# Kernel optimization log

Measured on AMD Instinct MI355X. Metric: run time of the kernel, lower is better.

Reference implementation:

```python
import jax, jax.numpy as jnp
import numpy as np

B, T, C, HS = 8, 4096, 1024, 128
BLOCK = 4096  # block_size; T == BLOCK here


def _pyr_mask(bs):
    # Faithful numpy translation of the torch 'pyr' buffer construction.
    h = bs // 2
    top = np.repeat(np.flip(np.tril(np.ones((h, h), np.float32)), axis=1), 2, axis=0)  # (bs, h)
    reps = np.array([2] * (h - 1) + [1])
    bot = np.concatenate(
        [np.zeros((1, h), np.float32),
         np.repeat(np.tril(np.ones((h, h), np.float32)), reps, axis=0)], axis=0)  # (bs, h)
    return np.concatenate([top, bot], axis=1)  # (bs, bs)


def setup_inputs() -> dict:
    key = jax.random.key(0)
    kx, kq, kk, kv = jax.random.split(key, 4)
    s = C ** -0.5
    x = jax.random.normal(kx, (B, T, C), jnp.float32)
    Wq = jax.random.normal(kq, (C, HS), jnp.float32) * s
    Wk = jax.random.normal(kk, (C, HS), jnp.float32) * s
    Wv = jax.random.normal(kv, (C, HS), jnp.float32) * s
    return {"x": x, "Wq": Wq, "Wk": Wk, "Wv": Wv}


def reference(x, Wq, Wk, Wv):
    Tlen = x.shape[1]
    start = (BLOCK - Tlen) // 2
    end = BLOCK + (-(BLOCK - Tlen)) // 2  # python floor-div, matches torch slicing
    mask = jnp.asarray(_pyr_mask(BLOCK)[:Tlen, start:end])  # (T, T) 0/1

    q = x @ Wq  # (B, T, HS)
    k = x @ Wk
    v = x @ Wv
    wei = jnp.einsum('btd,bsd->bts', q, k) * (HS ** -0.5)  # (B, T, T)
    wei = jnp.where(mask == 0, -jnp.inf, wei)  # bidirectional_mode == 'bi'
    wei = jax.nn.softmax(wei, axis=-1)
    # dropout p=0.0 -> identity
    return wei @ v  # (B, T, HS)
```

## Files before the change

### kernel.cpp

```cpp
#include <hip/hip_runtime.h>

typedef unsigned short u16;
typedef __attribute__((ext_vector_type(8))) short bf16x8;
typedef __attribute__((ext_vector_type(8))) unsigned short u16x8;
typedef __attribute__((ext_vector_type(4))) float f32x4;
typedef __attribute__((ext_vector_type(4))) unsigned short u16x4;

#define Bn 8
#define Tn 4096
#define Cn 1024
#define HSn 128

__device__ __forceinline__ float bf2f(u16 b) {
    unsigned u = ((unsigned)b) << 16;
    return __builtin_bit_cast(float, u);
}
__device__ __forceinline__ u16 f2bf(float f) {
    unsigned u = __builtin_bit_cast(unsigned, f);
    unsigned r = (u + 0x7fffu + ((u >> 16) & 1u)) >> 16;
    return (u16)r;
}

extern "C" __global__ __launch_bounds__(256) void head_wtrans(
    const float* __restrict__ Wq, const float* __restrict__ Wk,
    const float* __restrict__ Wv, u16* __restrict__ wt) {
    const float* W = (blockIdx.y == 0) ? Wq : (blockIdx.y == 1) ? Wk : Wv;
    const float scale =
        (blockIdx.y == 0) ? (0.08838834764831845f * 1.4426950408889634f) : 1.0f;
    u16* o = wt + (size_t)blockIdx.y * Cn * HSn;
    int tid = blockIdx.x * 256 + threadIdx.x;
    int n = tid >> 10, kk = tid & 1023;
    o[tid] = f2bf(W[kk * HSn + n] * scale);
}

extern "C" __global__ __launch_bounds__(256, 1) void head_proj(
    const float* __restrict__ x, const u16* __restrict__ wt, u16* __restrict__ qo,
    u16* __restrict__ ko, u16* __restrict__ vto) {
    __shared__ __align__(16) u16 aL[128 * 40];
    __shared__ __align__(16) u16 bL[3 * 128 * 40];
    const int tid = threadIdx.x;
    const int w = tid >> 6, l = tid & 63, quad = l >> 4, ln = l & 15;
    const int bm0 = blockIdx.x * 128;

    const f32x4 zero4 = {0.f, 0.f, 0.f, 0.f};
    f32x4 acc[3][4][4];
#pragma unroll
    for (int s = 0; s < 3; s++)
#pragma unroll
        for (int i = 0; i < 4; i++)
#pragma unroll
            for (int j = 0; j < 4; j++) acc[s][i][j] = zero4;

    const int m0w = (w & 1) * 64, n0w = (w >> 1) * 64;

    f32x4 xp[4];
    u16x8 wp[3][2];
    const int xrow[4] = {tid >> 3, (256 + tid) >> 3, (512 + tid) >> 3, (768 + tid) >> 3};
    const int xch = tid & 7;
    const int wrow[2] = {tid >> 2, (256 + tid) >> 2};
    const int wch = tid & 3;

#pragma unroll
    for (int p = 0; p < 4; p++)
        xp[p] = *(const f32x4*)(x + ((size_t)(bm0 + xrow[p])) * Cn + xch * 4);
#pragma unroll
    for (int s = 0; s < 3; s++)
#pragma unroll
        for (int p = 0; p < 2; p++)
            wp[s][p] = *(const u16x8*)(wt + (size_t)s * Cn * HSn + (size_t)wrow[p] * Cn +
                                       wch * 8);

    for (int kt = 0; kt < Cn / 32; kt++) {
        __syncthreads();
#pragma unroll
        for (int p = 0; p < 4; p++) {
            u16x4 vb;
#pragma unroll
            for (int j = 0; j < 4; j++) vb[j] = f2bf(xp[p][j]);
            *(u16x4*)(aL + xrow[p] * 40 + xch * 4) = vb;
        }
#pragma unroll
        for (int s = 0; s < 3; s++)
#pragma unroll
            for (int p = 0; p < 2; p++)
                *(u16x8*)(bL + s * 5120 + wrow[p] * 40 + wch * 8) = wp[s][p];
        if (kt + 1 < Cn / 32) {
            const int kn = (kt + 1) * 32;
#pragma unroll
            for (int p = 0; p < 4; p++)
                xp[p] = *(const f32x4*)(x + ((size_t)(bm0 + xrow[p])) * Cn + kn + xch * 4);
#pragma unroll
            for (int s = 0; s < 3; s++)
#pragma unroll
                for (int p = 0; p < 2; p++)
                    wp[s][p] = *(const u16x8*)(wt + (size_t)s * Cn * HSn +
                                               (size_t)wrow[p] * Cn + kn + wch * 8);
        }
        __syncthreads();
        bf16x8 af[4];
#pragma unroll
        for (int mi = 0; mi < 4; mi++)
            af[mi] = *(const bf16x8*)(aL + (m0w + mi * 16 + ln) * 40 + quad * 8);
#pragma unroll
        for (int s = 0; s < 3; s++) {
            bf16x8 bf[4];
#pragma unroll
            for (int ni = 0; ni < 4; ni++)
                bf[ni] =
                    *(const bf16x8*)(bL + s * 5120 + (n0w + ni * 16 + ln) * 40 + quad * 8);
#pragma unroll
            for (int mi = 0; mi < 4; mi++)
#pragma unroll
                for (int ni = 0; ni < 4; ni++)
                    acc[s][mi][ni] = __builtin_amdgcn_mfma_f32_16x16x32_bf16(
                        af[mi], bf[ni], acc[s][mi][ni], 0, 0, 0);
        }
    }
#pragma unroll
    for (int mi = 0; mi < 4; mi++)
#pragma unroll
        for (int ni = 0; ni < 4; ni++)
#pragma unroll
            for (int r = 0; r < 4; r++) {
                int grow = bm0 + m0w + mi * 16 + quad * 4 + r;
                int col = n0w + ni * 16 + ln;
                qo[(size_t)grow * HSn + col] = f2bf(acc[0][mi][ni][r]);
                ko[(size_t)grow * HSn + col] = f2bf(acc[1][mi][ni][r]);
                int bb = grow >> 12, t = grow & 4095;
                vto[((size_t)bb * HSn + col) * Tn + t] = f2bf(acc[2][mi][ni][r]);
            }
}


extern "C" __global__ __launch_bounds__(256) void head_flash_chunk(
    const u16* __restrict__ q, const u16* __restrict__ k, const u16* __restrict__ vt,
    u16* __restrict__ Opart, float* __restrict__ ml) {
    __shared__ __align__(16) u16 kL[64 * 136];
    __shared__ __align__(16) u16 vL[128 * 72];
    __shared__ __align__(16) u16 pL[4 * 16 * 72];
    const int tid = threadIdx.x;
    const int w = tid >> 6, l = tid & 63, quad = l >> 4, ln = l & 15;
    const int cid = blockIdx.x;
    const int qb = 63 - (cid >> 4);
    const int b = (cid & 15) >> 1;
    const int half = cid & 1;
    const int q0 = qb * 64;
    const int qrow = q0 + w * 16;

    const int rkBase = tid >> 4, ckK = tid & 15;
    const int rvBase = tid >> 3, ckV = tid & 7;

    bf16x8 qf[4];
#pragma unroll
    for (int ks = 0; ks < 4; ks++)
        qf[ks] = *(const bf16x8*)(q + ((size_t)b * Tn + qrow + ln) * HSn + ks * 32 +
                                  quad * 8);

    const f32x4 zero4 = {0.f, 0.f, 0.f, 0.f};
    float m2 = -1e30f, l2 = 0.f;
    const int qme = qrow + ln;
    const int clo = 2047 - (qme >> 1), chi = 2047 + ((qme + 1) >> 1);
    f32x4 o[8];
#pragma unroll
    for (int dt = 0; dt < 8; dt++) o[dt] = zero4;

    const int qmax = q0 + 63;
    const int tlo = (2047 - (qmax >> 1)) >> 6;
    const int thi = (2047 + ((qmax + 1) >> 1)) >> 6;
    const int W = thi - tlo + 1;
    const int c0 = (W + 1) >> 1;
    const int kstart = half ? tlo + c0 : tlo;
    const int kend = half ? thi : tlo + c0 - 1;

    u16x8 pk[4], pv[4];
    {
        const int t0 = kstart * 64;
#pragma unroll
        for (int p = 0; p < 4; p++)
            pk[p] = *(const u16x8*)(k + ((size_t)b * Tn + t0 + p * 16 + rkBase) * HSn +
                                    ckK * 8);
#pragma unroll
        for (int p = 0; p < 4; p++)
            pv[p] = *(const u16x8*)(vt + ((size_t)b * HSn + p * 32 + rvBase) * Tn + t0 +
                                    ckV * 8);
    }

    for (int kt = kstart; kt <= kend; kt++) {
        const int t0 = kt * 64;
        __syncthreads();
#pragma unroll
        for (int p = 0; p < 4; p++)
            *(u16x8*)(kL + (p * 16 + rkBase) * 136 + ckK * 8) = pk[p];
#pragma unroll
        for (int p = 0; p < 4; p++)
            *(u16x8*)(vL + (p * 32 + rvBase) * 72 + ckV * 8) = pv[p];
        if (kt < kend) {
            const int t1 = t0 + 64;
#pragma unroll
            for (int p = 0; p < 4; p++)
                pk[p] = *(const u16x8*)(k + ((size_t)b * Tn + t1 + p * 16 + rkBase) * HSn +
                                        ckK * 8);
#pragma unroll
            for (int p = 0; p < 4; p++)
                pv[p] = *(const u16x8*)(vt + ((size_t)b * HSn + p * 32 + rvBase) * Tn +
                                        t1 + ckV * 8);
        }
        __syncthreads();

        f32x4 s[4];
#pragma unroll
        for (int nt = 0; nt < 4; nt++) s[nt] = zero4;
#pragma unroll
        for (int nt = 0; nt < 4; nt++) {
            int R = nt * 16 + ln;
#pragma unroll
            for (int ks = 0; ks < 4; ks++) {
                bf16x8 kf = *(const bf16x8*)(kL + R * 136 + (ks * 4 + quad) * 8);
                s[nt] = __builtin_amdgcn_mfma_f32_16x16x32_bf16(kf, qf[ks], s[nt], 0, 0, 0);
            }
        }
#pragma unroll
        for (int nt = 0; nt < 4; nt++)
#pragma unroll
            for (int r = 0; r < 4; r++) {
                int t = t0 + nt * 16 + quad * 4 + r;
                bool valid = (t >= clo) && (t <= chi);
                s[nt][r] = valid ? s[nt][r] : -1e30f;
            }
        float mc = s[0][0];
#pragma unroll
        for (int nt = 0; nt < 4; nt++)
#pragma unroll
            for (int r = 0; r < 4; r++) mc = fmaxf(mc, s[nt][r]);
        mc = fmaxf(mc, __shfl_xor(mc, 16, 64));
        mc = fmaxf(mc, __shfl_xor(mc, 32, 64));
        float mn = fmaxf(m2, mc);
        float alpha = exp2f(m2 - mn);
        m2 = mn;
        float ls = 0.f;
#pragma unroll
        for (int nt = 0; nt < 4; nt++) {
            u16x4 pb4;
#pragma unroll
            for (int r = 0; r < 4; r++) {
                float pvx = exp2f(s[nt][r] - mn);
                u16 pb = f2bf(pvx);
                ls += bf2f(pb);
                pb4[r] = pb;
            }
            *(u16x4*)(pL + w * 1152 + ln * 72 + nt * 16 + quad * 4) = pb4;
        }
        ls += __shfl_xor(ls, 16, 64);
        ls += __shfl_xor(ls, 32, 64);
        l2 = l2 * alpha + ls;
        float aR[4];
#pragma unroll
        for (int r = 0; r < 4; r++) aR[r] = __shfl(alpha, quad * 4 + r, 64);
#pragma unroll
        for (int dt = 0; dt < 8; dt++) {
            f32x4 oo = o[dt];
#pragma unroll
            for (int r = 0; r < 4; r++) oo[r] *= aR[r];
            o[dt] = oo;
        }
#pragma unroll
        for (int jt = 0; jt < 2; jt++) {
            bf16x8 pf = *(const bf16x8*)(pL + w * 1152 + ln * 72 + jt * 32 + quad * 8);
#pragma unroll
            for (int dt = 0; dt < 8; dt++) {
                int R = dt * 16 + ln;
                bf16x8 vf = *(const bf16x8*)(vL + R * 72 + (jt * 4 + quad) * 8);
                o[dt] = __builtin_amdgcn_mfma_f32_16x16x32_bf16(pf, vf, o[dt], 0, 0, 0);
            }
        }
    }
#pragma unroll
    for (int dt = 0; dt < 8; dt++)
#pragma unroll
        for (int r = 0; r < 4; r++)
            Opart[((size_t)cid * 64 + w * 16 + quad * 4 + r) * HSn + dt * 16 + ln] =
                f2bf(o[dt][r]);
    if (l < 16) {
        ml[((size_t)cid * 64 + w * 16 + ln) * 2 + 0] = m2;
        ml[((size_t)cid * 64 + w * 16 + ln) * 2 + 1] = l2;
    }
}

extern "C" __global__ __launch_bounds__(256) void head_combine(
    const u16* __restrict__ Opart, const float* __restrict__ ml,
    float* __restrict__ out) {
    const int bid = blockIdx.x;
    const int qb = bid >> 3, b = bid & 7;
    const int tid = threadIdx.x;
    const int row = tid >> 2, dseg = (tid & 3) * 32;
    const int cid0 = (63 - qb) * 16 + b * 2;
    const size_t r0 = (size_t)cid0 * 64 + row, r1 = r0 + 64;
    float m0 = ml[r0 * 2], l0 = ml[r0 * 2 + 1];
    float m1 = ml[r1 * 2], l1 = ml[r1 * 2 + 1];
    float ms = fmaxf(m0, m1);
    float w0 = exp2f(m0 - ms), w1 = exp2f(m1 - ms);
    float inv = 1.0f / (w0 * l0 + w1 * l1);
    float* op = out + ((size_t)b * Tn + qb * 64 + row) * HSn + dseg;
    const u16* p0 = Opart + r0 * HSn + dseg;
    const u16* p1 = Opart + r1 * HSn + dseg;
#pragma unroll
    for (int j = 0; j < 4; j++) {
        u16x8 a = *(const u16x8*)(p0 + j * 8);
        u16x8 c = *(const u16x8*)(p1 + j * 8);
        f32x4 o1, o2;
#pragma unroll
        for (int e = 0; e < 4; e++) o1[e] = (w0 * bf2f(a[e]) + w1 * bf2f(c[e])) * inv;
#pragma unroll
        for (int e = 0; e < 4; e++) o2[e] = (w0 * bf2f(a[4 + e]) + w1 * bf2f(c[4 + e])) * inv;
        *(f32x4*)(op + j * 8) = o1;
        *(f32x4*)(op + j * 8 + 4) = o2;
    }
}

extern "C" __global__ __launch_bounds__(256) void head_flash(
    const u16* __restrict__ q, const u16* __restrict__ k, const u16* __restrict__ vt,
    float* __restrict__ out) {
    __shared__ __align__(16) u16 kL[64 * 136];
    __shared__ __align__(16) u16 vL[128 * 72];
    __shared__ __align__(16) u16 pL[4 * 16 * 72];
    const int tid = threadIdx.x;
    const int w = tid >> 6, l = tid & 63, quad = l >> 4, ln = l & 15;
    const int bx = blockIdx.x;
    const int half = bx >> 8, idx = bx & 255;
    const int p5 = idx & 31, b = idx >> 5;
    const int qb = half ? p5 : 63 - p5;
    const int q0 = qb * 64;
    const int qrow = q0 + w * 16;
    const int rkBase = tid >> 4, ckK = tid & 15;
    const int rvBase = tid >> 3, ckV = tid & 7;

    bf16x8 qf[4];
#pragma unroll
    for (int ks = 0; ks < 4; ks++)
        qf[ks] = *(const bf16x8*)(q + ((size_t)b * Tn + qrow + ln) * HSn + ks * 32 +
                                  quad * 8);
    const f32x4 zero4 = {0.f, 0.f, 0.f, 0.f};
    float m2 = -1e30f, l2 = 0.f;
    const int qme = qrow + ln;
    const int clo = 2047 - (qme >> 1), chi = 2047 + ((qme + 1) >> 1);
    f32x4 o[8];
#pragma unroll
    for (int dt = 0; dt < 8; dt++) o[dt] = zero4;
    const int qmax = q0 + 63;
    const int tlo = (2047 - (qmax >> 1)) >> 6;
    const int thi = (2047 + ((qmax + 1) >> 1)) >> 6;

    u16x8 pk[4], pv[4];
    {
        const int t0 = tlo * 64;
#pragma unroll
        for (int p = 0; p < 4; p++)
            pk[p] = *(const u16x8*)(k + ((size_t)b * Tn + t0 + p * 16 + rkBase) * HSn +
                                    ckK * 8);
#pragma unroll
        for (int p = 0; p < 4; p++)
            pv[p] = *(const u16x8*)(vt + ((size_t)b * HSn + p * 32 + rvBase) * Tn + t0 +
                                    ckV * 8);
    }
    for (int kt = tlo; kt <= thi; kt++) {
        const int t0 = kt * 64;
        __syncthreads();
#pragma unroll
        for (int p = 0; p < 4; p++)
            *(u16x8*)(kL + (p * 16 + rkBase) * 136 + ckK * 8) = pk[p];
#pragma unroll
        for (int p = 0; p < 4; p++)
            *(u16x8*)(vL + (p * 32 + rvBase) * 72 + ckV * 8) = pv[p];
        if (kt < thi) {
            const int t1 = t0 + 64;
#pragma unroll
            for (int p = 0; p < 4; p++)
                pk[p] = *(const u16x8*)(k + ((size_t)b * Tn + t1 + p * 16 + rkBase) * HSn +
                                        ckK * 8);
#pragma unroll
            for (int p = 0; p < 4; p++)
                pv[p] = *(const u16x8*)(vt + ((size_t)b * HSn + p * 32 + rvBase) * Tn +
                                        t1 + ckV * 8);
        }
        __syncthreads();
        f32x4 s[4];
#pragma unroll
        for (int nt = 0; nt < 4; nt++) s[nt] = zero4;
#pragma unroll
        for (int nt = 0; nt < 4; nt++) {
            int R = nt * 16 + ln;
#pragma unroll
            for (int ks = 0; ks < 4; ks++) {
                bf16x8 kf = *(const bf16x8*)(kL + R * 136 + (ks * 4 + quad) * 8);
                s[nt] = __builtin_amdgcn_mfma_f32_16x16x32_bf16(kf, qf[ks], s[nt], 0, 0, 0);
            }
        }
#pragma unroll
        for (int nt = 0; nt < 4; nt++)
#pragma unroll
            for (int r = 0; r < 4; r++) {
                int t = t0 + nt * 16 + quad * 4 + r;
                bool valid = (t >= clo) && (t <= chi);
                s[nt][r] = valid ? s[nt][r] : -1e30f;
            }
        float mc = s[0][0];
#pragma unroll
        for (int nt = 0; nt < 4; nt++)
#pragma unroll
            for (int r = 0; r < 4; r++) mc = fmaxf(mc, s[nt][r]);
        mc = fmaxf(mc, __shfl_xor(mc, 16, 64));
        mc = fmaxf(mc, __shfl_xor(mc, 32, 64));
        float mn = fmaxf(m2, mc);
        float alpha = exp2f(m2 - mn);
        m2 = mn;
        float ls = 0.f;
#pragma unroll
        for (int nt = 0; nt < 4; nt++) {
            u16x4 pb4;
#pragma unroll
            for (int r = 0; r < 4; r++) {
                float pvx = exp2f(s[nt][r] - mn);
                u16 pb = f2bf(pvx);
                ls += bf2f(pb);
                pb4[r] = pb;
            }
            *(u16x4*)(pL + w * 1152 + ln * 72 + nt * 16 + quad * 4) = pb4;
        }
        ls += __shfl_xor(ls, 16, 64);
        ls += __shfl_xor(ls, 32, 64);
        l2 = l2 * alpha + ls;
        float aR[4];
#pragma unroll
        for (int r = 0; r < 4; r++) aR[r] = __shfl(alpha, quad * 4 + r, 64);
#pragma unroll
        for (int dt = 0; dt < 8; dt++) {
            f32x4 oo = o[dt];
#pragma unroll
            for (int r = 0; r < 4; r++) oo[r] *= aR[r];
            o[dt] = oo;
        }
#pragma unroll
        for (int jt = 0; jt < 2; jt++) {
            bf16x8 pf = *(const bf16x8*)(pL + w * 1152 + ln * 72 + jt * 32 + quad * 8);
#pragma unroll
            for (int dt = 0; dt < 8; dt++) {
                int R = dt * 16 + ln;
                bf16x8 vf = *(const bf16x8*)(vL + R * 72 + (jt * 4 + quad) * 8);
                o[dt] = __builtin_amdgcn_mfma_f32_16x16x32_bf16(pf, vf, o[dt], 0, 0, 0);
            }
        }
    }
    float inv = 1.0f / l2;
    float rl[4];
#pragma unroll
    for (int r = 0; r < 4; r++) rl[r] = __shfl(inv, quad * 4 + r, 64);
#pragma unroll
    for (int dt = 0; dt < 8; dt++)
#pragma unroll
        for (int r = 0; r < 4; r++) {
            int row = qrow + quad * 4 + r;
            out[((size_t)b * Tn + row) * HSn + dt * 16 + ln] = o[dt][r] * rl[r];
        }
}

extern "C" void kernel_launch(void* const* d_in, const int* in_sizes, int n_in,
                              void* d_out, int out_size, void* d_ws, size_t ws_size,
                              hipStream_t stream) {
    const float* x = (const float*)d_in[0];
    const float* Wq = (const float*)d_in[1];
    const float* Wk = (const float*)d_in[2];
    const float* Wv = (const float*)d_in[3];
    float* outp = (float*)d_out;
    char* ws = (char*)d_ws;
    u16* wt = (u16*)(ws);
    u16* qb = (u16*)(ws + (1u << 20));
    u16* kb = (u16*)(ws + (9u << 20));
    u16* vtb = (u16*)(ws + (17u << 20));
    u16* Opart = (u16*)(ws + (25u << 20));
    float* ml = (float*)(ws + (42u << 20));

    head_wtrans<<<dim3(512, 3), 256, 0, stream>>>(Wq, Wk, Wv, wt);
    head_proj<<<dim3(256), 256, 0, stream>>>(x, wt, qb, kb, vtb);
    if (ws_size >= (44ull << 20)) {
        head_flash_chunk<<<dim3(1024), 256, 0, stream>>>(qb, kb, vtb, Opart, ml);
        head_combine<<<dim3(512), 256, 0, stream>>>(Opart, ml, outp);
    } else {
        head_flash<<<dim3(512), 256, 0, stream>>>(qb, kb, vtb, outp);
    }
}
```

Baseline: 326.7 us.

## Use packed bf16 converts, skip dead key tiles, lazy rescale, and MFMA priority

```diff
diff --git a/kernel.cpp b/kernel.cpp
--- a/kernel.cpp
+++ b/kernel.cpp
@@ -5,6 +5,7 @@
 typedef __attribute__((ext_vector_type(8))) unsigned short u16x8;
 typedef __attribute__((ext_vector_type(4))) float f32x4;
 typedef __attribute__((ext_vector_type(4))) unsigned short u16x4;
+typedef __attribute__((ext_vector_type(2))) unsigned int u32x2;
 
 #define Bn 8
 #define Tn 4096
@@ -15,11 +16,12 @@
     unsigned u = ((unsigned)b) << 16;
     return __builtin_bit_cast(float, u);
 }
-__device__ __forceinline__ u16 f2bf(float f) {
-    unsigned u = __builtin_bit_cast(unsigned, f);
-    unsigned r = (u + 0x7fffu + ((u >> 16) & 1u)) >> 16;
-    return (u16)r;
-}
+__device__ __forceinline__ unsigned cvt_pk_bf16(float a, float b) {
+    unsigned r;
+    asm("v_cvt_pk_bf16_f32 %0, %1, %2" : "=v"(r) : "v"(a), "v"(b));
+    return r;
+}
+__device__ __forceinline__ u16 f2bf(float f) { return (u16)cvt_pk_bf16(f, f); }
 
 extern "C" __global__ __launch_bounds__(256) void head_wtrans(
     const float* __restrict__ Wq, const float* __restrict__ Wk,
@@ -74,10 +76,10 @@
         __syncthreads();
 #pragma unroll
         for (int p = 0; p < 4; p++) {
-            u16x4 vb;
-#pragma unroll
-            for (int j = 0; j < 4; j++) vb[j] = f2bf(xp[p][j]);
-            *(u16x4*)(aL + xrow[p] * 40 + xch * 4) = vb;
+            u32x2 d;
+            d.x = cvt_pk_bf16(xp[p][0], xp[p][1]);
+            d.y = cvt_pk_bf16(xp[p][2], xp[p][3]);
+            *(u32x2*)(aL + xrow[p] * 40 + xch * 4) = d;
         }
 #pragma unroll
         for (int s = 0; s < 3; s++)
@@ -130,7 +132,6 @@
                 vto[((size_t)bb * HSn + col) * Tn + t] = f2bf(acc[2][mi][ni][r]);
             }
 }
-
 
 extern "C" __global__ __launch_bounds__(256) void head_flash_chunk(
     const u16* __restrict__ q, const u16* __restrict__ k, const u16* __restrict__ vt,
@@ -160,6 +161,10 @@
     float m2 = -1e30f, l2 = 0.f;
     const int qme = qrow + ln;
     const int clo = 2047 - (qme >> 1), chi = 2047 + ((qme + 1) >> 1);
+    const int cloW0 = 2047 - (qrow >> 1);
+    const int chiW0 = 2047 + ((qrow + 1) >> 1);
+    const int cloMin = 2047 - ((qrow + 15) >> 1);
+    const int chiMax = 2047 + ((qrow + 16) >> 1);
     f32x4 o[8];
 #pragma unroll
     for (int dt = 0; dt < 8; dt++) o[dt] = zero4;
@@ -207,9 +212,13 @@
         }
         __syncthreads();
 
+        const bool deadTile = (t0 + 63 < cloMin) || (t0 > chiMax);
+        if (deadTile) continue;
+
         f32x4 s[4];
 #pragma unroll
         for (int nt = 0; nt < 4; nt++) s[nt] = zero4;
+        __builtin_amdgcn_s_setprio(1);
 #pragma unroll
         for (int nt = 0; nt < 4; nt++) {
             int R = nt * 16 + ln;
@@ -219,14 +228,17 @@
                 s[nt] = __builtin_amdgcn_mfma_f32_16x16x32_bf16(kf, qf[ks], s[nt], 0, 0, 0);
             }
         }
-#pragma unroll
-        for (int nt = 0; nt < 4; nt++)
-#pragma unroll
-            for (int r = 0; r < 4; r++) {
-                int t = t0 + nt * 16 + quad * 4 + r;
-                bool valid = (t >= clo) && (t <= chi);
-                s[nt][r] = valid ? s[nt][r] : -1e30f;
-            }
+        __builtin_amdgcn_s_setprio(0);
+        if (t0 < cloW0 || t0 + 63 > chiW0) {
+#pragma unroll
+            for (int nt = 0; nt < 4; nt++)
+#pragma unroll
+                for (int r = 0; r < 4; r++) {
+                    int t = t0 + nt * 16 + quad * 4 + r;
+                    bool valid = (t >= clo) && (t <= chi);
+                    s[nt][r] = valid ? s[nt][r] : -1e30f;
+                }
+        }
         float mc = s[0][0];
 #pragma unroll
         for (int nt = 0; nt < 4; nt++)
@@ -234,35 +246,42 @@
             for (int r = 0; r < 4; r++) mc = fmaxf(mc, s[nt][r]);
         mc = fmaxf(mc, __shfl_xor(mc, 16, 64));
         mc = fmaxf(mc, __shfl_xor(mc, 32, 64));
-        float mn = fmaxf(m2, mc);
-        float alpha = exp2f(m2 - mn);
-        m2 = mn;
+        const bool growm = !__all(mc - m2 <= 8.0f);
+        float mn = m2, alpha = 1.0f;
+        if (growm) {
+            mn = fmaxf(m2, mc);
+            alpha = exp2f(m2 - mn);
+            m2 = mn;
+        }
         float ls = 0.f;
 #pragma unroll
         for (int nt = 0; nt < 4; nt++) {
-            u16x4 pb4;
-#pragma unroll
-            for (int r = 0; r < 4; r++) {
-                float pvx = exp2f(s[nt][r] - mn);
-                u16 pb = f2bf(pvx);
-                ls += bf2f(pb);
-                pb4[r] = pb;
-            }
-            *(u16x4*)(pL + w * 1152 + ln * 72 + nt * 16 + quad * 4) = pb4;
+            float p0 = exp2f(s[nt][0] - mn), p1 = exp2f(s[nt][1] - mn);
+            float p2 = exp2f(s[nt][2] - mn), p3 = exp2f(s[nt][3] - mn);
+            ls += (p0 + p1) + (p2 + p3);
+            u32x2 d;
+            d.x = cvt_pk_bf16(p0, p1);
+            d.y = cvt_pk_bf16(p2, p3);
+            *(u32x2*)(pL + w * 1152 + ln * 72 + nt * 16 + quad * 4) = d;
         }
         ls += __shfl_xor(ls, 16, 64);
         ls += __shfl_xor(ls, 32, 64);
-        l2 = l2 * alpha + ls;
-        float aR[4];
-#pragma unroll
-        for (int r = 0; r < 4; r++) aR[r] = __shfl(alpha, quad * 4 + r, 64);
-#pragma unroll
-        for (int dt = 0; dt < 8; dt++) {
-            f32x4 oo = o[dt];
-#pragma unroll
-            for (int r = 0; r < 4; r++) oo[r] *= aR[r];
-            o[dt] = oo;
-        }
+        if (growm) {
+            l2 = l2 * alpha + ls;
+            float aR[4];
+#pragma unroll
+            for (int r = 0; r < 4; r++) aR[r] = __shfl(alpha, quad * 4 + r, 64);
+#pragma unroll
+            for (int dt = 0; dt < 8; dt++) {
+                f32x4 oo = o[dt];
+#pragma unroll
+                for (int r = 0; r < 4; r++) oo[r] *= aR[r];
+                o[dt] = oo;
+            }
+        } else {
+            l2 += ls;
+        }
+        __builtin_amdgcn_s_setprio(1);
 #pragma unroll
         for (int jt = 0; jt < 2; jt++) {
             bf16x8 pf = *(const bf16x8*)(pL + w * 1152 + ln * 72 + jt * 32 + quad * 8);
@@ -273,6 +292,7 @@
                 o[dt] = __builtin_amdgcn_mfma_f32_16x16x32_bf16(pf, vf, o[dt], 0, 0, 0);
             }
         }
+        __builtin_amdgcn_s_setprio(0);
     }
 #pragma unroll
     for (int dt = 0; dt < 8; dt++)
@@ -416,15 +436,13 @@
         float ls = 0.f;
 #pragma unroll
         for (int nt = 0; nt < 4; nt++) {
-            u16x4 pb4;
-#pragma unroll
-            for (int r = 0; r < 4; r++) {
-                float pvx = exp2f(s[nt][r] - mn);
-                u16 pb = f2bf(pvx);
-                ls += bf2f(pb);
-                pb4[r] = pb;
-            }
-            *(u16x4*)(pL + w * 1152 + ln * 72 + nt * 16 + quad * 4) = pb4;
+            float p0 = exp2f(s[nt][0] - mn), p1 = exp2f(s[nt][1] - mn);
+            float p2 = exp2f(s[nt][2] - mn), p3 = exp2f(s[nt][3] - mn);
+            ls += (p0 + p1) + (p2 + p3);
+            u32x2 d;
+            d.x = cvt_pk_bf16(p0, p1);
+            d.y = cvt_pk_bf16(p2, p3);
+            *(u32x2*)(pL + w * 1152 + ln * 72 + nt * 16 + quad * 4) = d;
         }
         ls += __shfl_xor(ls, 16, 64);
         ls += __shfl_xor(ls, 32, 64);
```

After: 309.8 us. -5.1%, faster.
